# Optimization experiments

Measured on AMD Instinct MI355X. Metric: run time of the kernel, lower is better.

The kernel has to match this reference:

```python
import jax, jax.numpy as jnp
import numpy as np

NEG = -1e30  # safe stand-in for -inf in fp32


def _seg_logsumexp(scores, seg, num_segments):
    m = jax.ops.segment_max(scores, seg, num_segments=num_segments)
    m = jnp.maximum(m, NEG)
    s = jax.ops.segment_sum(jnp.exp(scores - m[seg]), seg, num_segments=num_segments)
    return jnp.where(s > 0, m + jnp.log(s), NEG)


def _chain_ll(x, length, src, dst, pdf, logw, init_lp, final_lp):
    # Log-domain HMM forward recursion over an edge-list graph.
    # x: [T, D] log-likelihoods; returns scalar log total path weight.
    S = init_lp.shape[0]
    T = x.shape[0]

    def step(alpha, inputs):
        xt, t = inputs
        scores = alpha[src] + logw + xt[pdf]          # [E]
        new_alpha = _seg_logsumexp(scores, dst, S)    # [S]
        alpha = jnp.where(t < length, new_alpha, alpha)
        return alpha, None

    alpha, _ = jax.lax.scan(step, init_lp, (x, jnp.arange(T)))
    return jax.nn.logsumexp(alpha + final_lp)


def chain_loss(x, x_lengths, den_src, den_dst, den_pdf, den_logw, den_init, den_final,
               num_src, num_dst, num_pdf, num_logw, num_init, num_final):
    # Denominator: one shared graph for all batch elements.
    den_ll = jax.vmap(_chain_ll, in_axes=(0, 0, None, None, None, None, None, None))(
        x, x_lengths, den_src, den_dst, den_pdf, den_logw, den_init, den_final)
    # Numerator: one graph per utterance.
    num_ll = jax.vmap(_chain_ll)(
        x, x_lengths, num_src, num_dst, num_pdf, num_logw, num_init, num_final)
    den_objf = jnp.sum(den_ll)
    num_objf = jnp.sum(num_ll)
    objf = -(num_objf - den_objf)
    return objf / jnp.sum(x_lengths).astype(x.dtype)  # avg=True


def setup_inputs() -> dict:
    key = jax.random.key(0)
    ks = jax.random.split(key, 16)
    B, T, D = 32, 500, 3072
    S_den, E_den = 4000, 120000
    S_num, E_num = 200, 600

    x = jax.random.normal(ks[0], (B, T, D), dtype=jnp.float32)
    x_lengths = jnp.sort(jax.random.randint(ks[1], (B,), T // 2, T + 1, dtype=jnp.int32))[::-1]

    den_src = jax.random.randint(ks[2], (E_den,), 0, S_den, dtype=jnp.int32)
    den_dst = jax.random.randint(ks[3], (E_den,), 0, S_den, dtype=jnp.int32)
    den_pdf = jax.random.randint(ks[4], (E_den,), 0, D, dtype=jnp.int32)
    den_logw = -5.0 * jax.random.uniform(ks[5], (E_den,), dtype=jnp.float32)
    den_init = -3.0 * jax.random.uniform(ks[6], (S_den,), dtype=jnp.float32)
    den_final = -3.0 * jax.random.uniform(ks[7], (S_den,), dtype=jnp.float32)

    num_src = jax.random.randint(ks[8], (B, E_num), 0, S_num, dtype=jnp.int32)
    num_dst = jax.random.randint(ks[9], (B, E_num), 0, S_num, dtype=jnp.int32)
    num_pdf = jax.random.randint(ks[10], (B, E_num), 0, D, dtype=jnp.int32)
    num_logw = -5.0 * jax.random.uniform(ks[11], (B, E_num), dtype=jnp.float32)
    num_init = -3.0 * jax.random.uniform(ks[12], (B, S_num), dtype=jnp.float32)
    num_final = -3.0 * jax.random.uniform(ks[13], (B, S_num), dtype=jnp.float32)

    return {"x": x, "x_lengths": x_lengths,
            "den_src": den_src, "den_dst": den_dst, "den_pdf": den_pdf,
            "den_logw": den_logw, "den_init": den_init, "den_final": den_final,
            "num_src": num_src, "num_dst": num_dst, "num_pdf": num_pdf,
            "num_logw": num_logw, "num_init": num_init, "num_final": num_final}


def reference(x, x_lengths, den_src, den_dst, den_pdf, den_logw, den_init, den_final,
              num_src, num_dst, num_pdf, num_logw, num_init, num_final):
    return chain_loss(x, x_lengths, den_src, den_dst, den_pdf, den_logw, den_init, den_final,
                      num_src, num_dst, num_pdf, num_logw, num_init, num_final)
```

## Files before the change

### kernel.cpp

```cpp
#include <hip/hip_runtime.h>

constexpr int B_     = 32;
constexpr int T_     = 500;
constexpr int D_     = 3072;
constexpr int S_DEN  = 4000;
constexpr int E_DEN  = 120000;
constexpr int S_NUM  = 200;
constexpr int E_NUM  = 600;
constexpr int NCHUNK = 8;
constexpr int WTGT   = (E_DEN + 2 * E_NUM) / NCHUNK;
constexpr int ECAP   = 15488;
constexpr int NTB    = 512;

__global__ void zero_ints(int* p, int n) {
    int i = blockIdx.x * 256 + threadIdx.x;
    if (i < n) p[i] = 0;
}

__global__ void hist_den(const int* __restrict__ dst, int* __restrict__ cnt) {
    int e = blockIdx.x * 256 + threadIdx.x;
    if (e < E_DEN) atomicAdd(&cnt[dst[e]], 1);
}

__global__ void hist_num(const int* __restrict__ dst, int* __restrict__ cnt) {
    int b = blockIdx.y, j = blockIdx.x * 256 + threadIdx.x;
    if (j < E_NUM) atomicAdd(&cnt[b * S_NUM + dst[b * E_NUM + j]], 1);
}

__global__ void scan_den(int* __restrict__ cnt_cur, int* __restrict__ row) {
    __shared__ int part[1024];
    int tid = threadIdx.x, base = tid * 4;
    int c[4], pre[4], s = 0;
    #pragma unroll
    for (int j = 0; j < 4; ++j) {
        int idx = base + j;
        c[j] = (idx < S_DEN) ? cnt_cur[idx] : 0;
        pre[j] = s; s += c[j];
    }
    part[tid] = s; __syncthreads();
    for (int off = 1; off < 1024; off <<= 1) {
        int v = (tid >= off) ? part[tid - off] : 0; __syncthreads();
        part[tid] += v; __syncthreads();
    }
    int offs = (tid > 0) ? part[tid - 1] : 0;
    #pragma unroll
    for (int j = 0; j < 4; ++j) {
        int idx = base + j;
        if (idx < S_DEN) { row[idx] = offs + pre[j]; cnt_cur[idx] = offs + pre[j]; }
    }
    if (tid == 1023) row[S_DEN] = part[1023];
}

__global__ void scan_num(int* __restrict__ cnt_cur, int* __restrict__ row) {
    __shared__ int part[256];
    int b = blockIdx.x, tid = threadIdx.x;
    int c = (tid < S_NUM) ? cnt_cur[b * S_NUM + tid] : 0;
    part[tid] = c; __syncthreads();
    for (int off = 1; off < 256; off <<= 1) {
        int v = (tid >= off) ? part[tid - off] : 0; __syncthreads();
        part[tid] += v; __syncthreads();
    }
    int excl = part[tid] - c;
    if (tid < S_NUM) { row[b * (S_NUM + 1) + tid] = excl; cnt_cur[b * S_NUM + tid] = excl; }
    if (tid == 255) row[b * (S_NUM + 1) + S_NUM] = part[255];
}

__global__ void scatter_den(const int* __restrict__ src, const int* __restrict__ dst,
                            const int* __restrict__ pdf, const float* __restrict__ logw,
                            int* __restrict__ cur, int2* __restrict__ csr) {
    int e = blockIdx.x * 256 + threadIdx.x;
    if (e >= E_DEN) return;
    int pos = atomicAdd(&cur[dst[e]], 1);
    csr[pos] = make_int2(src[e] | (pdf[e] << 12), __float_as_int(__expf(logw[e])));
}

__global__ void scatter_num(const int* __restrict__ src, const int* __restrict__ dst,
                            const int* __restrict__ pdf, const float* __restrict__ logw,
                            int* __restrict__ cur, int2* __restrict__ csr) {
    int b = blockIdx.y, j = blockIdx.x * 256 + threadIdx.x;
    if (j >= E_NUM) return;
    int e = b * E_NUM + j;
    int pos = atomicAdd(&cur[b * S_NUM + dst[e]], 1);
    csr[b * E_NUM + pos] = make_int2(src[e] | (pdf[e] << 12), __float_as_int(__expf(logw[e])));
}

__global__ void part_den(const int* __restrict__ row, int* __restrict__ part) {
    int r = threadIdx.x;
    if (r > NCHUNK) return;
    if (r == 0)        { part[0] = 0; return; }
    if (r == NCHUNK)   { part[NCHUNK] = S_DEN; return; }
    int target = r * WTGT; if (target > E_DEN) target = E_DEN;
    int lo = 0, hi = S_DEN;
    while (lo < hi) { int mid = (lo + hi) >> 1; if (row[mid] < target) lo = mid + 1; else hi = mid; }
    part[r] = lo;
}

__global__ __launch_bounds__(NTB, 1)
void chain_persist(const float* __restrict__ x, const int* __restrict__ x_lengths,
                   const int* __restrict__ den_row, const int2* __restrict__ den_csr,
                   const int* __restrict__ part,
                   const int* __restrict__ num_row, const int2* __restrict__ num_csr,
                   const float* __restrict__ den_init, const float* __restrict__ den_final,
                   const float* __restrict__ num_init, const float* __restrict__ num_final,
                   unsigned long long* __restrict__ EAslot,
                   unsigned long long* __restrict__ Fflag,
                   float* __restrict__ ll) {
    __shared__ int2   csr_d[ECAP];
    __shared__ float4 ex4[D_ / 4];
    __shared__ float  eal[S_DEN];
    __shared__ int2   csr_n[E_NUM];
    __shared__ float  eal_n[S_NUM];
    __shared__ float  red[8], red_n[8];
    float* ex = (float*)ex4;

    const int tid = threadIdx.x;
    const int b   = blockIdx.x & 31;
    const int r   = blockIdx.x >> 5;
    const int len = x_lengths[b];

    const int s0 = part[r], s1 = part[r + 1];
    const int e0 = den_row[s0], e1 = den_row[s1];
    const int ne = e1 - e0;
    for (int i = tid; i < ne; i += NTB) csr_d[i] = den_csr[e0 + i];
    const int sa = s0 + tid, sb = s0 + tid + NTB;
    int ba = 0, eaA = 0, bb = 0, ebB = 0;
    if (sa < s1) { ba = den_row[sa] - e0; eaA = den_row[sa + 1] - e0; }
    if (sb < s1) { bb = den_row[sb] - e0; ebB = den_row[sb + 1] - e0; }
    for (int s = tid; s < S_DEN; s += NTB) eal[s] = __expf(den_init[s]);

    int nb = 0, neE = 0;
    if (r == NCHUNK - 1) {
        for (int i = tid; i < E_NUM; i += NTB) csr_n[i] = num_csr[b * E_NUM + i];
        if (tid < S_NUM) {
            nb  = num_row[b * (S_NUM + 1) + tid];
            neE = num_row[b * (S_NUM + 1) + tid + 1];
            eal_n[tid] = __expf(num_init[b * S_NUM + tid]);
        }
    }

    const float* xb = x + (size_t)b * T_ * D_;
    const bool  has2 = tid < (D_ / 4 - NTB);
    float4 xr0, xr1;
    {
        const float4* p = (const float4*)xb;
        xr0 = p[tid];
        xr1 = has2 ? p[tid + NTB] : make_float4(0.f, 0.f, 0.f, 0.f);
        float4 ev;
        ev.x = __expf(fminf(xr0.x, 60.f)); ev.y = __expf(fminf(xr0.y, 60.f));
        ev.z = __expf(fminf(xr0.z, 60.f)); ev.w = __expf(fminf(xr0.w, 60.f));
        ex4[tid] = ev;
        if (has2) {
            float4 e1v;
            e1v.x = __expf(fminf(xr1.x, 60.f)); e1v.y = __expf(fminf(xr1.y, 60.f));
            e1v.z = __expf(fminf(xr1.z, 60.f)); e1v.w = __expf(fminf(xr1.w, 60.f));
            ex4[tid + NTB] = e1v;
        }
        if (len > 1) {
            const float4* pn = (const float4*)(xb + (size_t)D_);
            xr0 = pn[tid];
            if (has2) xr1 = pn[tid + NTB];
        }
    }
    __syncthreads();

    float off = 0.f, offn = 0.f, acc0 = 0.f, acc1 = 0.f, accn = 0.f;
    float inv_prev = 1.f;

    for (int t = 0; t < len; ++t) {
        float raw0 = 0.f, raw1 = 0.f;
        if (sa < s1) {
            float a0 = 0.f, a1 = 0.f;
            int e = ba;
            for (; e + 2 <= eaA; e += 2) {
                int2 p0 = csr_d[e], p1 = csr_d[e + 1];
                a0 += eal[p0.x & 0xFFF] * __int_as_float(p0.y) * ex[p0.x >> 12];
                a1 += eal[p1.x & 0xFFF] * __int_as_float(p1.y) * ex[p1.x >> 12];
            }
            if (e < eaA) {
                int2 p0 = csr_d[e];
                a0 += eal[p0.x & 0xFFF] * __int_as_float(p0.y) * ex[p0.x >> 12];
            }
            raw0 = a0 + a1;
        }
        if (sb < s1) {
            float a0 = 0.f, a1 = 0.f;
            int e = bb;
            for (; e + 2 <= ebB; e += 2) {
                int2 p0 = csr_d[e], p1 = csr_d[e + 1];
                a0 += eal[p0.x & 0xFFF] * __int_as_float(p0.y) * ex[p0.x >> 12];
                a1 += eal[p1.x & 0xFFF] * __int_as_float(p1.y) * ex[p1.x >> 12];
            }
            if (e < ebB) {
                int2 p0 = csr_d[e];
                a0 += eal[p0.x & 0xFFF] * __int_as_float(p0.y) * ex[p0.x >> 12];
            }
            raw1 = a0 + a1;
        }
        acc0 = raw0 * inv_prev;
        acc1 = raw1 * inv_prev;

        if (t + 1 < len) {
            unsigned long long* slw = EAslot + ((size_t)(t & 1) * B_ + b) * S_DEN;
            const unsigned long long tg = (unsigned long long)(unsigned)(t + 1) << 32;
            if (sa < s1)
                __hip_atomic_store(&slw[sa], tg | __float_as_uint(acc0),
                                   __ATOMIC_RELAXED, __HIP_MEMORY_SCOPE_AGENT);
            if (sb < s1)
                __hip_atomic_store(&slw[sb], tg | __float_as_uint(acc1),
                                   __ATOMIC_RELAXED, __HIP_MEMORY_SCOPE_AGENT);
        }

        float lmax_n = 0.f;
        if (r == NCHUNK - 1) {
            if (tid < S_NUM) {
                float a = 0.f;
                for (int e = nb; e < neE; ++e) {
                    int2 p0 = csr_n[e];
                    a += eal_n[p0.x & 0xFFF] * __int_as_float(p0.y) * ex[p0.x >> 12];
                }
                accn = a; lmax_n = a;
            }
            #pragma unroll
            for (int o = 32; o > 0; o >>= 1) lmax_n = fmaxf(lmax_n, __shfl_down(lmax_n, o));
            if ((tid & 63) == 0) red_n[tid >> 6] = lmax_n;
        }
        __syncthreads();

        if (r == NCHUNK - 1) {
            float Mn = red_n[0];
            #pragma unroll
            for (int w = 1; w < 8; ++w) Mn = fmaxf(Mn, red_n[w]);
            if (!(Mn > 0.f)) Mn = 1.f;
            if (tid < S_NUM) eal_n[tid] = accn / Mn;
            offn += __logf(Mn);
        }

        if (t + 1 < len) {
            float4 ev;
            ev.x = __expf(fminf(xr0.x, 60.f)); ev.y = __expf(fminf(xr0.y, 60.f));
            ev.z = __expf(fminf(xr0.z, 60.f)); ev.w = __expf(fminf(xr0.w, 60.f));
            ex4[tid] = ev;
            if (has2) {
                float4 e1v;
                e1v.x = __expf(fminf(xr1.x, 60.f)); e1v.y = __expf(fminf(xr1.y, 60.f));
                e1v.z = __expf(fminf(xr1.z, 60.f)); e1v.w = __expf(fminf(xr1.w, 60.f));
                ex4[tid + NTB] = e1v;
            }
            if (t + 2 < len) {
                const float4* pn = (const float4*)(xb + (size_t)(t + 2) * D_);
                xr0 = pn[tid];
                if (has2) xr1 = pn[tid + NTB];
            }

            const unsigned long long* slr = EAslot + ((size_t)(t & 1) * B_ + b) * S_DEN;
            const unsigned want = (unsigned)(t + 1);
            float mv = 0.f;
            unsigned rdy = 0;
            while (rdy != 0xFFu) {
                #pragma unroll
                for (int k = 0; k < 8; ++k) {
                    if (rdy & (1u << k)) continue;
                    int s = tid + k * NTB;
                    if (s >= S_DEN) { rdy |= 1u << k; continue; }
                    unsigned long long v = __hip_atomic_load(&slr[s],
                                             __ATOMIC_RELAXED, __HIP_MEMORY_SCOPE_AGENT);
                    if ((unsigned)(v >> 32) == want) {
                        float f = __uint_as_float((unsigned)v);
                        eal[s] = f;
                        mv = fmaxf(mv, f);
                        rdy |= 1u << k;
                    }
                }
                if (rdy != 0xFFu) __builtin_amdgcn_s_sleep(1);
            }
            #pragma unroll
            for (int o = 32; o > 0; o >>= 1) mv = fmaxf(mv, __shfl_down(mv, o));
            if ((tid & 63) == 0) red[tid >> 6] = mv;
            __syncthreads();

            float M = red[0];
            #pragma unroll
            for (int w = 1; w < 8; ++w) M = fmaxf(M, red[w]);
            if (!(M > 0.f)) M = 1.f;
            off += __logf(M);
            inv_prev = 1.f / M;
        }
    }

    float fs = 0.f;
    if (sa < s1) fs += acc0 * __expf(den_final[sa]);
    if (sb < s1) fs += acc1 * __expf(den_final[sb]);
    #pragma unroll
    for (int o = 32; o > 0; o >>= 1) fs += __shfl_down(fs, o);
    if ((tid & 63) == 0) red[tid >> 6] = fs;
    __syncthreads();

    if (tid == 0) {
        float bf = 0.f;
        #pragma unroll
        for (int w = 0; w < 8; ++w) bf += red[w];
        unsigned long long pv = ((unsigned long long)(unsigned)len << 32) |
                                (unsigned long long)__float_as_uint(bf);
        __hip_atomic_store(&Fflag[b * 8 + r], pv, __ATOMIC_RELAXED, __HIP_MEMORY_SCOPE_AGENT);
    }

    if (r == 0 && tid < 64) {
        float sv = 0.f;
        bool rdy = (tid >= 8);
        const unsigned want = (unsigned)len;
        while (true) {
            if (!rdy) {
                unsigned long long v = __hip_atomic_load(&Fflag[b * 8 + tid],
                                         __ATOMIC_RELAXED, __HIP_MEMORY_SCOPE_AGENT);
                if ((unsigned)(v >> 32) == want) { rdy = true; sv = __uint_as_float((unsigned)v); }
            }
            if (__all(rdy)) break;
            __builtin_amdgcn_s_sleep(1);
        }
        #pragma unroll
        for (int o = 4; o > 0; o >>= 1) sv += __shfl_down(sv, o);
        if (tid == 0) ll[b] = __logf(sv) + off;
    }

    if (r == NCHUNK - 1) {
        float ns = (tid < S_NUM) ? eal_n[tid] * __expf(num_final[b * S_NUM + tid]) : 0.f;
        #pragma unroll
        for (int o = 32; o > 0; o >>= 1) ns += __shfl_down(ns, o);
        if ((tid & 63) == 0) red_n[tid >> 6] = ns;
        __syncthreads();
        if (tid == 0) {
            float tn = 0.f;
            #pragma unroll
            for (int w = 0; w < 8; ++w) tn += red_n[w];
            ll[B_ + b] = __logf(tn) + offn;
        }
    }
}

__global__ void finalize_loss(const float* __restrict__ ll, const int* __restrict__ x_lengths,
                              float* __restrict__ out) {
    int tid = threadIdx.x;
    float d = (tid < B_) ? ll[tid] : 0.f;
    float n = (tid < B_) ? ll[B_ + tid] : 0.f;
    float l = (tid < B_) ? (float)x_lengths[tid] : 0.f;
    #pragma unroll
    for (int o = 32; o > 0; o >>= 1) {
        d += __shfl_down(d, o); n += __shfl_down(n, o); l += __shfl_down(l, o);
    }
    if (tid == 0) out[0] = (d - n) / l;
}

__global__ __launch_bounds__(1024)
void chain_forward_atomic(const float* __restrict__ x, const int* __restrict__ x_lengths,
                          const int* __restrict__ den_src, const int* __restrict__ den_dst,
                          const int* __restrict__ den_pdf, const float* __restrict__ den_logw,
                          const float* __restrict__ den_init, const float* __restrict__ den_final,
                          const int* __restrict__ num_src, const int* __restrict__ num_dst,
                          const int* __restrict__ num_pdf, const float* __restrict__ num_logw,
                          const float* __restrict__ num_init, const float* __restrict__ num_final,
                          float* __restrict__ ll_out) {
    __shared__ float ea[S_DEN];
    __shared__ float ssum[S_DEN];
    __shared__ float ex[D_];
    __shared__ float red[16];
    __shared__ float s_m;
    const int  tid = threadIdx.x;
    const bool is_den = blockIdx.x < B_;
    const int  b = is_den ? blockIdx.x : blockIdx.x - B_;
    const int  S = is_den ? S_DEN : S_NUM;
    const int  E = is_den ? E_DEN : E_NUM;
    const int*   esrc = is_den ? den_src : num_src + b * E_NUM;
    const int*   edst = is_den ? den_dst : num_dst + b * E_NUM;
    const int*   epdf = is_den ? den_pdf : num_pdf + b * E_NUM;
    const float* elw  = is_den ? den_logw: num_logw + b * E_NUM;
    const float* init = is_den ? den_init : num_init + b * S_NUM;
    const float* fin  = is_den ? den_final: num_final + b * S_NUM;
    const int    len  = x_lengths[b];
    const float* xb   = x + (size_t)b * T_ * D_;
    for (int s = tid; s < S; s += 1024) { ea[s] = __expf(init[s]); ssum[s] = 0.f; }
    float off = 0.f;
    for (int t = 0; t < len; ++t) {
        const float4* xr4 = reinterpret_cast<const float4*>(xb + (size_t)t * D_);
        for (int d = tid; d < D_ / 4; d += 1024) {
            float4 v = xr4[d];
            ex[4*d+0] = __expf(fminf(v.x, 60.f)); ex[4*d+1] = __expf(fminf(v.y, 60.f));
            ex[4*d+2] = __expf(fminf(v.z, 60.f)); ex[4*d+3] = __expf(fminf(v.w, 60.f));
        }
        __syncthreads();
        for (int e = tid; e < E; e += 1024)
            unsafeAtomicAdd(&ssum[edst[e]], ea[esrc[e]] * __expf(elw[e]) * ex[epdf[e]]);
        __syncthreads();
        float lm = 0.f;
        for (int s = tid; s < S; s += 1024) lm = fmaxf(lm, ssum[s]);
        #pragma unroll
        for (int o = 32; o > 0; o >>= 1) lm = fmaxf(lm, __shfl_down(lm, o));
        if ((tid & 63) == 0) red[tid >> 6] = lm;
        __syncthreads();
        if (tid == 0) {
            float m = red[0];
            for (int w = 1; w < 16; ++w) m = fmaxf(m, red[w]);
            s_m = (m > 0.f) ? m : 1.f;
        }
        __syncthreads();
        float inv = 1.f / s_m;
        off += __logf(s_m);
        for (int s = tid; s < S; s += 1024) { ea[s] = ssum[s] * inv; ssum[s] = 0.f; }
    }
    float lsum = 0.f;
    for (int s = tid; s < S; s += 1024) lsum += ea[s] * __expf(fin[s]);
    #pragma unroll
    for (int o = 32; o > 0; o >>= 1) lsum += __shfl_down(lsum, o);
    if ((tid & 63) == 0) red[tid >> 6] = lsum;
    __syncthreads();
    if (tid == 0) {
        float tot = 0.f;
        for (int w = 0; w < 16; ++w) tot += red[w];
        ll_out[blockIdx.x] = off + __logf(tot);
    }
}

static inline size_t align16(size_t v) { return (v + 15) & ~size_t(15); }

extern "C" void kernel_launch(void* const* d_in, const int* in_sizes, int n_in,
                              void* d_out, int out_size, void* d_ws, size_t ws_size,
                              hipStream_t stream) {
    const float* x         = (const float*)d_in[0];
    const int*   x_lengths = (const int*)  d_in[1];
    const int*   den_src   = (const int*)  d_in[2];
    const int*   den_dst   = (const int*)  d_in[3];
    const int*   den_pdf   = (const int*)  d_in[4];
    const float* den_logw  = (const float*)d_in[5];
    const float* den_init  = (const float*)d_in[6];
    const float* den_final = (const float*)d_in[7];
    const int*   num_src   = (const int*)  d_in[8];
    const int*   num_dst   = (const int*)  d_in[9];
    const int*   num_pdf   = (const int*)  d_in[10];
    const float* num_logw  = (const float*)d_in[11];
    const float* num_init  = (const float*)d_in[12];
    const float* num_final = (const float*)d_in[13];

    char* ws = (char*)d_ws;
    size_t o = 0;
    float*              ll      = (float*)             (ws + o); o = align16(o + 64 * sizeof(float));
    int*                den_row = (int*)               (ws + o); o = align16(o + (S_DEN + 1) * sizeof(int));
    int*                den_cur = (int*)               (ws + o); o = align16(o + S_DEN * sizeof(int));
    int*                num_row = (int*)               (ws + o); o = align16(o + B_ * (S_NUM + 1) * sizeof(int));
    int*                num_cur = (int*)               (ws + o); o = align16(o + B_ * S_NUM * sizeof(int));
    int2*               den_csr = (int2*)              (ws + o); o = align16(o + (size_t)E_DEN * sizeof(int2));
    int2*               num_csr = (int2*)              (ws + o); o = align16(o + (size_t)B_ * E_NUM * sizeof(int2));
    int*                part    = (int*)               (ws + o); o = align16(o + (NCHUNK + 1) * sizeof(int));
    unsigned long long* EAslot  = (unsigned long long*)(ws + o); o = align16(o + (size_t)2 * B_ * S_DEN * sizeof(unsigned long long));
    unsigned long long* Fflag   = (unsigned long long*)(ws + o); o = align16(o + (size_t)B_ * 8 * sizeof(unsigned long long));
    const size_t need = o;

    if (ws_size >= need) {
        zero_ints<<<(S_DEN + 255) / 256, 256, 0, stream>>>(den_cur, S_DEN);
        zero_ints<<<(B_ * S_NUM + 255) / 256, 256, 0, stream>>>(num_cur, B_ * S_NUM);
        hist_den<<<(E_DEN + 255) / 256, 256, 0, stream>>>(den_dst, den_cur);
        hist_num<<<dim3(3, B_), 256, 0, stream>>>(num_dst, num_cur);
        scan_den<<<1, 1024, 0, stream>>>(den_cur, den_row);
        scan_num<<<B_, 256, 0, stream>>>(num_cur, num_row);
        scatter_den<<<(E_DEN + 255) / 256, 256, 0, stream>>>(
            den_src, den_dst, den_pdf, den_logw, den_cur, den_csr);
        scatter_num<<<dim3(3, B_), 256, 0, stream>>>(
            num_src, num_dst, num_pdf, num_logw, num_cur, num_csr);
        part_den<<<1, 16, 0, stream>>>(den_row, part);

        void* args[] = {
            (void*)&x, (void*)&x_lengths, (void*)&den_row, (void*)&den_csr, (void*)&part,
            (void*)&num_row, (void*)&num_csr, (void*)&den_init, (void*)&den_final,
            (void*)&num_init, (void*)&num_final, (void*)&EAslot,
            (void*)&Fflag, (void*)&ll
        };
        hipError_t err = hipLaunchCooperativeKernel((const void*)chain_persist,
                                                    dim3(B_ * NCHUNK), dim3(NTB),
                                                    args, 0, stream);
        if (err != hipSuccess) {
            chain_persist<<<dim3(B_ * NCHUNK), dim3(NTB), 0, stream>>>(
                x, x_lengths, den_row, den_csr, part, num_row, num_csr,
                den_init, den_final, num_init, num_final,
                EAslot, Fflag, ll);
        }
        finalize_loss<<<1, 64, 0, stream>>>(ll, x_lengths, (float*)d_out);
    } else {
        chain_forward_atomic<<<2 * B_, 1024, 0, stream>>>(
            x, x_lengths, den_src, den_dst, den_pdf, den_logw, den_init, den_final,
            num_src, num_dst, num_pdf, num_logw, num_init, num_final, ll);
        finalize_loss<<<1, 64, 0, stream>>>(ll, x_lengths, (float*)d_out);
    }
}
```

Baseline: 3.385 ms.

## Double-buffer alpha and emission tables to drop one barrier per timestep

Double-buffers the shared alpha, emission-exp and numerator alpha arrays by timestep parity. This removes the mid-step __syncthreads that separated the numerator normalization from the emission refresh, and the numerator max reduction now shares the single barrier with the denominator max. Edge weights are also stored in shared memory as fp16 in a separate array rather than packed int2, which cuts LDS footprint and read width. The fp16 weights lose precision in the log-likelihood, and the doubled buffers raise LDS usage.

```diff
diff --git a/kernel.cpp b/kernel.cpp
--- a/kernel.cpp
+++ b/kernel.cpp
@@ -1,4 +1,5 @@
 #include <hip/hip_runtime.h>
+#include <hip/hip_fp16.h>
 
 constexpr int B_     = 32;
 constexpr int T_     = 500;
@@ -105,13 +106,13 @@
                    unsigned long long* __restrict__ EAslot,
                    unsigned long long* __restrict__ Fflag,
                    float* __restrict__ ll) {
-    __shared__ int2   csr_d[ECAP];
-    __shared__ float4 ex4[D_ / 4];
-    __shared__ float  eal[S_DEN];
+    __shared__ int    csr_i[ECAP];
+    __shared__ __half csr_w[ECAP];
+    __shared__ float  ex2[2][D_];
+    __shared__ float  eal2[2][S_DEN];
     __shared__ int2   csr_n[E_NUM];
-    __shared__ float  eal_n[S_NUM];
-    __shared__ float  red[8], red_n[8];
-    float* ex = (float*)ex4;
+    __shared__ float  ealn2[2][S_NUM];
+    __shared__ float  red2[2][8], redn2[2][8];
 
     const int tid = threadIdx.x;
     const int b   = blockIdx.x & 31;
@@ -121,12 +122,16 @@
     const int s0 = part[r], s1 = part[r + 1];
     const int e0 = den_row[s0], e1 = den_row[s1];
     const int ne = e1 - e0;
-    for (int i = tid; i < ne; i += NTB) csr_d[i] = den_csr[e0 + i];
+    for (int i = tid; i < ne; i += NTB) {
+        int2 pk = den_csr[e0 + i];
+        csr_i[i] = pk.x;
+        csr_w[i] = __float2half_rn(__int_as_float(pk.y));
+    }
     const int sa = s0 + tid, sb = s0 + tid + NTB;
     int ba = 0, eaA = 0, bb = 0, ebB = 0;
     if (sa < s1) { ba = den_row[sa] - e0; eaA = den_row[sa + 1] - e0; }
     if (sb < s1) { bb = den_row[sb] - e0; ebB = den_row[sb + 1] - e0; }
-    for (int s = tid; s < S_DEN; s += NTB) eal[s] = __expf(den_init[s]);
+    for (int s = tid; s < S_DEN; s += NTB) eal2[0][s] = __expf(den_init[s]);
 
     int nb = 0, neE = 0;
     if (r == NCHUNK - 1) {
@@ -134,7 +139,7 @@
         if (tid < S_NUM) {
             nb  = num_row[b * (S_NUM + 1) + tid];
             neE = num_row[b * (S_NUM + 1) + tid + 1];
-            eal_n[tid] = __expf(num_init[b * S_NUM + tid]);
+            ealn2[0][tid] = __expf(num_init[b * S_NUM + tid]);
         }
     }
 
@@ -142,18 +147,18 @@
     const bool  has2 = tid < (D_ / 4 - NTB);
     float4 xr0, xr1;
     {
-        const float4* p = (const float4*)xb;
-        xr0 = p[tid];
-        xr1 = has2 ? p[tid + NTB] : make_float4(0.f, 0.f, 0.f, 0.f);
+        const float4* p4 = (const float4*)xb;
+        xr0 = p4[tid];
+        xr1 = has2 ? p4[tid + NTB] : make_float4(0.f, 0.f, 0.f, 0.f);
         float4 ev;
         ev.x = __expf(fminf(xr0.x, 60.f)); ev.y = __expf(fminf(xr0.y, 60.f));
         ev.z = __expf(fminf(xr0.z, 60.f)); ev.w = __expf(fminf(xr0.w, 60.f));
-        ex4[tid] = ev;
+        ((float4*)ex2[0])[tid] = ev;
         if (has2) {
             float4 e1v;
             e1v.x = __expf(fminf(xr1.x, 60.f)); e1v.y = __expf(fminf(xr1.y, 60.f));
             e1v.z = __expf(fminf(xr1.z, 60.f)); e1v.w = __expf(fminf(xr1.w, 60.f));
-            ex4[tid + NTB] = e1v;
+            ((float4*)ex2[0])[tid + NTB] = e1v;
         }
         if (len > 1) {
             const float4* pn = (const float4*)(xb + (size_t)D_);
@@ -163,44 +168,40 @@
     }
     __syncthreads();
 
+#define PROC_ROW(ebeg, eend, raw) do {                                          \
+        int e_ = (ebeg), en_ = (eend);                                          \
+        float a0_ = 0.f, a1_ = 0.f;                                             \
+        for (; e_ + 2 <= en_; e_ += 2) {                                        \
+            int   i0_ = csr_i[e_], i1_ = csr_i[e_ + 1];                         \
+            float w0_ = __half2float(csr_w[e_]);                                \
+            float w1_ = __half2float(csr_w[e_ + 1]);                            \
+            a0_ += EALP[i0_ & 0xFFF] * w0_ * EXP_[i0_ >> 12];                    \
+            a1_ += EALP[i1_ & 0xFFF] * w1_ * EXP_[i1_ >> 12];                    \
+        }                                                                       \
+        if (e_ < en_) {                                                         \
+            int   i0_ = csr_i[e_];                                              \
+            float w0_ = __half2float(csr_w[e_]);                                \
+            a0_ += EALP[i0_ & 0xFFF] * w0_ * EXP_[i0_ >> 12];                    \
+        }                                                                       \
+        raw += a0_ + a1_;                                                       \
+    } while (0)
+
     float off = 0.f, offn = 0.f, acc0 = 0.f, acc1 = 0.f, accn = 0.f;
-    float inv_prev = 1.f;
+    float inv_prev = 1.f, invn_prev = 1.f;
 
     for (int t = 0; t < len; ++t) {
+        const int p = t & 1, q = p ^ 1;
+        const float* EALP = eal2[p];
+        const float* EXP_ = ex2[p];
+
         float raw0 = 0.f, raw1 = 0.f;
-        if (sa < s1) {
-            float a0 = 0.f, a1 = 0.f;
-            int e = ba;
-            for (; e + 2 <= eaA; e += 2) {
-                int2 p0 = csr_d[e], p1 = csr_d[e + 1];
-                a0 += eal[p0.x & 0xFFF] * __int_as_float(p0.y) * ex[p0.x >> 12];
-                a1 += eal[p1.x & 0xFFF] * __int_as_float(p1.y) * ex[p1.x >> 12];
-            }
-            if (e < eaA) {
-                int2 p0 = csr_d[e];
-                a0 += eal[p0.x & 0xFFF] * __int_as_float(p0.y) * ex[p0.x >> 12];
-            }
-            raw0 = a0 + a1;
-        }
-        if (sb < s1) {
-            float a0 = 0.f, a1 = 0.f;
-            int e = bb;
-            for (; e + 2 <= ebB; e += 2) {
-                int2 p0 = csr_d[e], p1 = csr_d[e + 1];
-                a0 += eal[p0.x & 0xFFF] * __int_as_float(p0.y) * ex[p0.x >> 12];
-                a1 += eal[p1.x & 0xFFF] * __int_as_float(p1.y) * ex[p1.x >> 12];
-            }
-            if (e < ebB) {
-                int2 p0 = csr_d[e];
-                a0 += eal[p0.x & 0xFFF] * __int_as_float(p0.y) * ex[p0.x >> 12];
-            }
-            raw1 = a0 + a1;
-        }
+        if (sa < s1) PROC_ROW(ba, eaA, raw0);
+        if (sb < s1) PROC_ROW(bb, ebB, raw1);
         acc0 = raw0 * inv_prev;
         acc1 = raw1 * inv_prev;
 
         if (t + 1 < len) {
-            unsigned long long* slw = EAslot + ((size_t)(t & 1) * B_ + b) * S_DEN;
+            unsigned long long* slw = EAslot + ((size_t)p * B_ + b) * S_DEN;
             const unsigned long long tg = (unsigned long long)(unsigned)(t + 1) << 32;
             if (sa < s1)
                 __hip_atomic_store(&slw[sa], tg | __float_as_uint(acc0),
@@ -210,49 +211,37 @@
                                    __ATOMIC_RELAXED, __HIP_MEMORY_SCOPE_AGENT);
         }
 
-        float lmax_n = 0.f;
         if (r == NCHUNK - 1) {
+            float rawn = 0.f;
             if (tid < S_NUM) {
-                float a = 0.f;
                 for (int e = nb; e < neE; ++e) {
                     int2 p0 = csr_n[e];
-                    a += eal_n[p0.x & 0xFFF] * __int_as_float(p0.y) * ex[p0.x >> 12];
+                    rawn += ealn2[p][p0.x & 0xFFF] * __int_as_float(p0.y) * EXP_[p0.x >> 12];
                 }
-                accn = a; lmax_n = a;
-            }
-            #pragma unroll
-            for (int o = 32; o > 0; o >>= 1) lmax_n = fmaxf(lmax_n, __shfl_down(lmax_n, o));
-            if ((tid & 63) == 0) red_n[tid >> 6] = lmax_n;
-        }
-        __syncthreads();
-
-        if (r == NCHUNK - 1) {
-            float Mn = red_n[0];
-            #pragma unroll
-            for (int w = 1; w < 8; ++w) Mn = fmaxf(Mn, red_n[w]);
-            if (!(Mn > 0.f)) Mn = 1.f;
-            if (tid < S_NUM) eal_n[tid] = accn / Mn;
-            offn += __logf(Mn);
+            }
+            accn = rawn * invn_prev;
         }
 
         if (t + 1 < len) {
-            float4 ev;
-            ev.x = __expf(fminf(xr0.x, 60.f)); ev.y = __expf(fminf(xr0.y, 60.f));
-            ev.z = __expf(fminf(xr0.z, 60.f)); ev.w = __expf(fminf(xr0.w, 60.f));
-            ex4[tid] = ev;
-            if (has2) {
-                float4 e1v;
-                e1v.x = __expf(fminf(xr1.x, 60.f)); e1v.y = __expf(fminf(xr1.y, 60.f));
-                e1v.z = __expf(fminf(xr1.z, 60.f)); e1v.w = __expf(fminf(xr1.w, 60.f));
-                ex4[tid + NTB] = e1v;
-            }
-            if (t + 2 < len) {
-                const float4* pn = (const float4*)(xb + (size_t)(t + 2) * D_);
-                xr0 = pn[tid];
-                if (has2) xr1 = pn[tid + NTB];
-            }
-
-            const unsigned long long* slr = EAslot + ((size_t)(t & 1) * B_ + b) * S_DEN;
+            {
+                float4 ev;
+                ev.x = __expf(fminf(xr0.x, 60.f)); ev.y = __expf(fminf(xr0.y, 60.f));
+                ev.z = __expf(fminf(xr0.z, 60.f)); ev.w = __expf(fminf(xr0.w, 60.f));
+                ((float4*)ex2[q])[tid] = ev;
+                if (has2) {
+                    float4 e1v;
+                    e1v.x = __expf(fminf(xr1.x, 60.f)); e1v.y = __expf(fminf(xr1.y, 60.f));
+                    e1v.z = __expf(fminf(xr1.z, 60.f)); e1v.w = __expf(fminf(xr1.w, 60.f));
+                    ((float4*)ex2[q])[tid + NTB] = e1v;
+                }
+                if (t + 2 < len) {
+                    const float4* pn = (const float4*)(xb + (size_t)(t + 2) * D_);
+                    xr0 = pn[tid];
+                    if (has2) xr1 = pn[tid + NTB];
+                }
+            }
+
+            const unsigned long long* slr = EAslot + ((size_t)p * B_ + b) * S_DEN;
             const unsigned want = (unsigned)(t + 1);
             float mv = 0.f;
             unsigned rdy = 0;
@@ -266,7 +255,7 @@
                                              __ATOMIC_RELAXED, __HIP_MEMORY_SCOPE_AGENT);
                     if ((unsigned)(v >> 32) == want) {
                         float f = __uint_as_float((unsigned)v);
-                        eal[s] = f;
+                        eal2[q][s] = f;
                         mv = fmaxf(mv, f);
                         rdy |= 1u << k;
                     }
@@ -275,30 +264,54 @@
             }
             #pragma unroll
             for (int o = 32; o > 0; o >>= 1) mv = fmaxf(mv, __shfl_down(mv, o));
-            if ((tid & 63) == 0) red[tid >> 6] = mv;
+            if ((tid & 63) == 0) red2[p][tid >> 6] = mv;
+
+            if (r == NCHUNK - 1) {
+                if (tid < S_NUM) ealn2[q][tid] = accn;
+                float mvn = accn;
+                #pragma unroll
+                for (int o = 32; o > 0; o >>= 1) mvn = fmaxf(mvn, __shfl_down(mvn, o));
+                if ((tid & 63) == 0) redn2[p][tid >> 6] = mvn;
+            }
+
             __syncthreads();
 
-            float M = red[0];
+            float M = red2[p][0];
             #pragma unroll
-            for (int w = 1; w < 8; ++w) M = fmaxf(M, red[w]);
+            for (int w = 1; w < 8; ++w) M = fmaxf(M, red2[p][w]);
             if (!(M > 0.f)) M = 1.f;
             off += __logf(M);
             inv_prev = 1.f / M;
-        }
-    }
+            if (r == NCHUNK - 1) {
+                float Mn = redn2[p][0];
+                #pragma unroll
+                for (int w = 1; w < 8; ++w) Mn = fmaxf(Mn, redn2[p][w]);
+                if (!(Mn > 0.f)) Mn = 1.f;
+                offn += __logf(Mn);
+                invn_prev = 1.f / Mn;
+            }
+        }
+    }
+#undef PROC_ROW
 
     float fs = 0.f;
     if (sa < s1) fs += acc0 * __expf(den_final[sa]);
     if (sb < s1) fs += acc1 * __expf(den_final[sb]);
     #pragma unroll
     for (int o = 32; o > 0; o >>= 1) fs += __shfl_down(fs, o);
-    if ((tid & 63) == 0) red[tid >> 6] = fs;
+    if ((tid & 63) == 0) red2[0][tid >> 6] = fs;
+
+    float ns = (r == NCHUNK - 1 && tid < S_NUM)
+             ? accn * __expf(num_final[b * S_NUM + tid]) : 0.f;
+    #pragma unroll
+    for (int o = 32; o > 0; o >>= 1) ns += __shfl_down(ns, o);
+    if ((tid & 63) == 0) redn2[0][tid >> 6] = ns;
     __syncthreads();
 
     if (tid == 0) {
         float bf = 0.f;
         #pragma unroll
-        for (int w = 0; w < 8; ++w) bf += red[w];
+        for (int w = 0; w < 8; ++w) bf += red2[0][w];
         unsigned long long pv = ((unsigned long long)(unsigned)len << 32) |
                                 (unsigned long long)__float_as_uint(bf);
         __hip_atomic_store(&Fflag[b * 8 + r], pv, __ATOMIC_RELAXED, __HIP_MEMORY_SCOPE_AGENT);
@@ -322,18 +335,11 @@
         if (tid == 0) ll[b] = __logf(sv) + off;
     }
 
-    if (r == NCHUNK - 1) {
-        float ns = (tid < S_NUM) ? eal_n[tid] * __expf(num_final[b * S_NUM + tid]) : 0.f;
+    if (r == NCHUNK - 1 && tid == 0) {
+        float tn = 0.f;
         #pragma unroll
-        for (int o = 32; o > 0; o >>= 1) ns += __shfl_down(ns, o);
-        if ((tid & 63) == 0) red_n[tid >> 6] = ns;
-        __syncthreads();
-        if (tid == 0) {
-            float tn = 0.f;
-            #pragma unroll
-            for (int w = 0; w < 8; ++w) tn += red_n[w];
-            ll[B_ + b] = __logf(tn) + offn;
-        }
+        for (int w = 0; w < 8; ++w) tn += redn2[0][w];
+        ll[B_ + b] = __logf(tn) + offn;
     }
 }
 
```

New measurement: 4.683 ms. 1.38x slower.
